# Kernel tuning notes

Measured on AMD Instinct MI355X. Metric: run time of the kernel, lower is better.

## Reference

```python
import jax, jax.numpy as jnp
import numpy as np

F0_DIM, PH_DIM, MIDI_DIM, DUR_DIM = 64, 128, 64, 64
COND = 256
TOTAL = F0_DIM + PH_DIM + MIDI_DIM + DUR_DIM  # 320
EPS = 1e-5


def setup_inputs() -> dict:
    key = jax.random.key(0)
    ks = jax.random.split(key, 16)
    B, T = 16, 4096
    inp = {
        "f0": jax.random.uniform(ks[0], (B, T), jnp.float32) * 400.0 + 80.0,
        "phone": jax.random.randint(ks[1], (B, T), 0, 100, jnp.int32),
        "duration": jax.random.uniform(ks[2], (B, T), jnp.float32),
        "midi": jax.random.randint(ks[3], (B, T), 0, 128, jnp.int32),
        # f0 encoder: Linear(1,32) -> ReLU -> Linear(32,64)
        "f0_w1": jax.random.normal(ks[4], (1, F0_DIM // 2), jnp.float32) * 0.1,
        "f0_b1": jnp.zeros((F0_DIM // 2,), jnp.float32),
        "f0_w2": jax.random.normal(ks[5], (F0_DIM // 2, F0_DIM), jnp.float32) * 0.1,
        "f0_b2": jnp.zeros((F0_DIM,), jnp.float32),
        # embeddings
        "phone_table": jax.random.normal(ks[6], (100, PH_DIM), jnp.float32),
        "midi_table": jax.random.normal(ks[7], (128, MIDI_DIM), jnp.float32),
        # duration encoder: Linear(1,32) -> ReLU -> Linear(32,64)
        "dur_w1": jax.random.normal(ks[8], (1, DUR_DIM // 2), jnp.float32) * 0.1,
        "dur_b1": jnp.zeros((DUR_DIM // 2,), jnp.float32),
        "dur_w2": jax.random.normal(ks[9], (DUR_DIM // 2, DUR_DIM), jnp.float32) * 0.1,
        "dur_b2": jnp.zeros((DUR_DIM,), jnp.float32),
        # projection: Linear(320,256) -> LayerNorm(256) -> ReLU -> Linear(256,256)
        "proj_w1": jax.random.normal(ks[10], (TOTAL, COND), jnp.float32) * (1.0 / np.sqrt(TOTAL)),
        "proj_b1": jnp.zeros((COND,), jnp.float32),
        "ln_g": jnp.ones((COND,), jnp.float32),
        "ln_b": jnp.zeros((COND,), jnp.float32),
        "proj_w2": jax.random.normal(ks[11], (COND, COND), jnp.float32) * (1.0 / np.sqrt(COND)),
        "proj_b2": jnp.zeros((COND,), jnp.float32),
    }
    return inp


def reference(f0, phone, duration, midi,
              f0_w1, f0_b1, f0_w2, f0_b2,
              phone_table, midi_table,
              dur_w1, dur_b1, dur_w2, dur_b2,
              proj_w1, proj_b1, ln_g, ln_b, proj_w2, proj_b2):
    # f0 / duration MLPs, vectorized over all (batch, time) positions
    f0_h = jax.nn.relu(f0[..., None] * f0_w1[0] + f0_b1)            # [B,T,32]
    f0_emb = f0_h @ f0_w2 + f0_b2                                    # [B,T,64]
    dur_h = jax.nn.relu(duration[..., None] * dur_w1[0] + dur_b1)    # [B,T,32]
    dur_emb = dur_h @ dur_w2 + dur_b2                                # [B,T,64]
    phone_emb = phone_table[phone]                                   # [B,T,128]
    midi_emb = midi_table[midi]                                      # [B,T,64]
    combined = jnp.concatenate([f0_emb, phone_emb, midi_emb, dur_emb], axis=-1)  # [B,T,320]
    h = combined @ proj_w1 + proj_b1                                 # [B,T,256]
    mu = jnp.mean(h, axis=-1, keepdims=True)
    var = jnp.mean((h - mu) ** 2, axis=-1, keepdims=True)
    h = (h - mu) * jax.lax.rsqrt(var + EPS) * ln_g + ln_b
    h = jax.nn.relu(h)
    return h @ proj_w2 + proj_b2                                     # [B,T,256]
```

## Files before the change

### kernel.cpp

```cpp
#include <hip/hip_runtime.h>

typedef _Float16 f16x8 __attribute__((ext_vector_type(8)));
typedef float f32x4 __attribute__((ext_vector_type(4)));
typedef unsigned int u32x2 __attribute__((ext_vector_type(2)));

#define MROWS 65536
#define BM 32
#define NBLK (MROWS / BM)

#define B1F_OFF 0u
#define B2F_OFF 65536u
#define TP_OFF 196608u
#define TM_OFF 299008u
#define BC_OFF 430080u
#define WFD_OFF 431104u


__device__ __forceinline__ unsigned a2off(unsigned X) {
  return (X * 16u) ^ (X & 0x30u);
}

__global__ __launch_bounds__(256) void prep_tables(
    const float* __restrict__ f0_w2, const float* __restrict__ f0_b2,
    const float* __restrict__ ptab, const float* __restrict__ mtab,
    const float* __restrict__ dur_w2, const float* __restrict__ dur_b2,
    const float* __restrict__ W1, const float* __restrict__ pb1,
    float* __restrict__ wsf) {
  const int r = blockIdx.x, n = threadIdx.x;
  if (r < 64) {
    float s = 0.f;
    if (r < 32) {
      for (int j = 0; j < 64; ++j) s = fmaf(f0_w2[r * 64 + j], W1[j * 256 + n], s);
    } else {
      for (int j = 0; j < 64; ++j) s = fmaf(dur_w2[(r - 32) * 64 + j], W1[(256 + j) * 256 + n], s);
    }
    wsf[WFD_OFF / 4 + r * 256 + n] = s;
  } else if (r < 164) {
    const int p = r - 64;
    float s = 0.f;
    for (int j = 0; j < 128; ++j) s = fmaf(ptab[p * 128 + j], W1[(64 + j) * 256 + n], s);
    wsf[TP_OFF / 4 + p * 256 + n] = s;
  } else if (r < 292) {
    const int m = r - 164;
    float s = 0.f;
    for (int j = 0; j < 64; ++j) s = fmaf(mtab[m * 64 + j], W1[(192 + j) * 256 + n], s);
    wsf[TM_OFF / 4 + m * 256 + n] = s;
  } else {
    float s = pb1[n];
    for (int j = 0; j < 64; ++j) {
      s = fmaf(f0_b2[j], W1[j * 256 + n], s);
      s = fmaf(dur_b2[j], W1[(256 + j) * 256 + n], s);
    }
    wsf[BC_OFF / 4 + n] = s;
  }
}

__global__ __launch_bounds__(64) void prep_frags(const float* __restrict__ W2, char* __restrict__ ws) {
  const float* Wfd = (const float*)(ws + WFD_OFF);
  const int t = blockIdx.x;
  const int l = threadIdx.x;
  const int qq = l >> 4, c = l & 15;
  if (t < 32) {
    const int kt = t >> 4, nt = t & 15;
    const int col = (nt >> 2) * 64 + c * 4 + (nt & 3);
    f16x8 v;
#pragma unroll
    for (int e = 0; e < 8; ++e) {
      const int k = kt * 32 + 4 * qq + (e & 3) + 16 * (e >> 2);
      v[e] = (_Float16)Wfd[k * 256 + col];
    }
    *(f16x8*)(ws + B1F_OFF + (unsigned)((kt * 16 + nt) * 64 + l) * 16u) = v;
  } else {
    const int t2 = t - 32;
    const int kt = t2 >> 4, nt = t2 & 15;
    const int col = (nt >> 2) * 64 + c * 4 + (nt & 3);
    f16x8 v;
#pragma unroll
    for (int e = 0; e < 8; ++e) {
      const int k = kt * 32 + 4 * qq + (e & 3) + 16 * (e >> 2);
      v[e] = (_Float16)W2[k * 256 + col];
    }
    *(f16x8*)(ws + B2F_OFF + (unsigned)((kt * 16 + nt) * 64 + l) * 16u) = v;
  }
}

__global__ __launch_bounds__(256, 4) void cond_enc_main(
    const float* __restrict__ f0g, const int* __restrict__ phone,
    const float* __restrict__ durg, const int* __restrict__ midi,
    const float* __restrict__ f0_w1, const float* __restrict__ f0_b1,
    const float* __restrict__ dur_w1, const float* __restrict__ dur_b1,
    const float* __restrict__ ln_g, const float* __restrict__ ln_b,
    const float* __restrict__ pb2, const char* __restrict__ ws,
    float* __restrict__ out) {
  __shared__ __align__(16) unsigned char smem[16384 + 512];
  unsigned char* Pbuf = smem;
  float* partials = (float*)(smem + 16384);

  const int tid = threadIdx.x;
  const int l = tid & 63;
  const int w = tid >> 6;
  const int wi = w & 1;
  const int wh = w >> 1;
  const int q = l >> 4;
  const int c = l & 15;
  const int rowbase = blockIdx.x * BM;

  const float* Tp = (const float*)(ws + TP_OFF);
  const float* Tm = (const float*)(ws + TM_OFF);

  const int rl = l & 31;
  const float xf_all = f0g[rowbase + rl];
  const float xd_all = durg[rowbase + rl];
  const int ph_all = phone[rowbase + rl];
  const int md_all = midi[rowbase + rl];

  f16x8 a1[2];
  {
    const float xf = __shfl(xf_all, wi * 16 + c);
    const float xd = __shfl(xd_all, wi * 16 + c);
#pragma unroll
    for (int kh = 0; kh < 2; ++kh) {
      f16x8 v;
#pragma unroll
      for (int e = 0; e < 8; ++e) {
        const int ki = 4 * q + (e & 3) + 16 * (e >> 2);
        const float wv = kh ? dur_w1[ki] : f0_w1[ki];
        const float bv = kh ? dur_b1[ki] : f0_b1[ki];
        const float x = kh ? xd : xf;
        v[e] = (_Float16)fmaxf(fmaf(x, wv, bv), 0.f);
      }
      a1[kh] = v;
    }
  }

  const f32x4 zero4 = {0.f, 0.f, 0.f, 0.f};
  f32x4 acc[8];
#pragma unroll
  for (int j = 0; j < 8; ++j) acc[j] = zero4;
  {
    const f16x8* B1p = (const f16x8*)(ws + B1F_OFF);
#pragma unroll
    for (int kt = 0; kt < 2; ++kt) {
#pragma unroll
      for (int jc = 0; jc < 2; ++jc) {
        f16x8 bfr[4];
#pragma unroll
        for (int j = 0; j < 4; ++j) bfr[j] = B1p[(kt * 16 + wh * 8 + jc * 4 + j) * 64 + l];
#pragma unroll
        for (int j = 0; j < 4; ++j)
          acc[jc * 4 + j] = __builtin_amdgcn_mfma_f32_16x16x32_f16(a1[kt], bfr[j], acc[jc * 4 + j], 0, 0, 0);
      }
    }
  }

  const float* bcp = (const float*)(ws + BC_OFF);
#pragma unroll
  for (int r = 0; r < 4; ++r) {
    const int rrel = wi * 16 + q * 4 + r;
    const int ph = __shfl(ph_all, rrel);
    const int md = __shfl(md_all, rrel);
    float s = 0.f, ss = 0.f;
#pragma unroll
    for (int gl = 0; gl < 2; ++gl) {
      const int g = wh * 2 + gl;
      const f32x4 tp4 = *(const f32x4*)(Tp + ph * 256 + g * 64 + c * 4);
      const f32x4 tm4 = *(const f32x4*)(Tm + md * 256 + g * 64 + c * 4);
      const f32x4 bc4 = *(const f32x4*)(bcp + g * 64 + c * 4);
#pragma unroll
      for (int bq = 0; bq < 4; ++bq) {
        float v = acc[4 * gl + bq][r] + bc4[bq] + tp4[bq] + tm4[bq];
        acc[4 * gl + bq][r] = v;
        s += v;
        ss = fmaf(v, v, ss);
      }
    }
#pragma unroll
    for (int m = 1; m < 16; m <<= 1) {
      s += __shfl_xor(s, m, 64);
      ss += __shfl_xor(ss, m, 64);
    }
    if (c == 0) {
      partials[rrel * 4 + wh * 2 + 0] = s;
      partials[rrel * 4 + wh * 2 + 1] = ss;
    }
  }
  __syncthreads();

  const int lp_base = 16 * (c & 3);
  const unsigned hoff = (unsigned)((c >> 2) & 1) * 8u;
#pragma unroll
  for (int r = 0; r < 4; ++r) {
    const int rrel = wi * 16 + q * 4 + r;
    const f32x4 pr = *(const f32x4*)(partials + rrel * 4);
    const float s = pr[0] + pr[2];
    const float ss = pr[1] + pr[3];
    const float mu = s * (1.f / 256.f);
    const float var = fmaxf(ss * (1.f / 256.f) - mu * mu, 0.f);
    const float rstd = rsqrtf(var + 1e-5f);
#pragma unroll
    for (int gl = 0; gl < 2; ++gl) {
      const int g = wh * 2 + gl;
      const f32x4 g4 = *(const f32x4*)(ln_g + g * 64 + c * 4);
      const f32x4 lb4 = *(const f32x4*)(ln_b + g * 64 + c * 4);
      unsigned short hw[4];
#pragma unroll
      for (int bq = 0; bq < 4; ++bq) {
        float v = fmaf((acc[4 * gl + bq][r] - mu) * rstd, g4[bq], lb4[bq]);
        v = fmaxf(v, 0.f);
        hw[bq] = __builtin_bit_cast(unsigned short, (_Float16)v);
      }
      u32x2 pkt;
      pkt[0] = (unsigned)hw[0] | ((unsigned)hw[1] << 16);
      pkt[1] = (unsigned)hw[2] | ((unsigned)hw[3] << 16);
      const int kt = 2 * g + (c >> 3);
      const unsigned X = (unsigned)((kt * 2 + wi) * 64 + (q * 4 + r + lp_base));
      *(u32x2*)(Pbuf + a2off(X) + hoff) = pkt;
    }
  }
  __syncthreads();

  f32x4 acc2[2][4];
#pragma unroll
  for (int i = 0; i < 2; ++i)
#pragma unroll
    for (int j = 0; j < 4; ++j) acc2[i][j] = zero4;
  {
    const f16x8* B2p = (const f16x8*)(ws + B2F_OFF);
#pragma unroll
    for (int kt = 0; kt < 8; ++kt) {
      const f16x8 a0 = *(const f16x8*)(Pbuf + a2off((unsigned)((kt * 2 + 0) * 64 + l)));
      const f16x8 a1f = *(const f16x8*)(Pbuf + a2off((unsigned)((kt * 2 + 1) * 64 + l)));
      f16x8 bfr[4];
#pragma unroll
      for (int j = 0; j < 4; ++j) bfr[j] = B2p[(kt * 16 + w * 4 + j) * 64 + l];
#pragma unroll
      for (int j = 0; j < 4; ++j) {
        acc2[0][j] = __builtin_amdgcn_mfma_f32_16x16x32_f16(a0, bfr[j], acc2[0][j], 0, 0, 0);
        acc2[1][j] = __builtin_amdgcn_mfma_f32_16x16x32_f16(a1f, bfr[j], acc2[1][j], 0, 0, 0);
      }
    }
  }

  const f32x4 b24 = *(const f32x4*)(pb2 + w * 64 + c * 4);
#pragma unroll
  for (int i = 0; i < 2; ++i)
#pragma unroll
    for (int r = 0; r < 4; ++r) {
      const int grow = rowbase + i * 16 + q * 4 + r;
      f32x4 st;
#pragma unroll
      for (int j = 0; j < 4; ++j) st[j] = acc2[i][j][r] + b24[j];
      __builtin_nontemporal_store(st, (f32x4*)(out + grow * 256 + w * 64 + c * 4));
    }
}

extern "C" void kernel_launch(void* const* d_in, const int* in_sizes, int n_in,
                              void* d_out, int out_size, void* d_ws, size_t ws_size,
                              hipStream_t stream) {
  (void)in_sizes; (void)n_in; (void)out_size; (void)ws_size;
  const float* f0 = (const float*)d_in[0];
  const int* phone = (const int*)d_in[1];
  const float* dur = (const float*)d_in[2];
  const int* midi = (const int*)d_in[3];
  const float* f0_w1 = (const float*)d_in[4];
  const float* f0_b1 = (const float*)d_in[5];
  const float* f0_w2 = (const float*)d_in[6];
  const float* f0_b2 = (const float*)d_in[7];
  const float* ptab = (const float*)d_in[8];
  const float* mtab = (const float*)d_in[9];
  const float* dur_w1 = (const float*)d_in[10];
  const float* dur_b1 = (const float*)d_in[11];
  const float* dur_w2 = (const float*)d_in[12];
  const float* dur_b2 = (const float*)d_in[13];
  const float* W1 = (const float*)d_in[14];
  const float* pb1 = (const float*)d_in[15];
  const float* ln_g = (const float*)d_in[16];
  const float* ln_b = (const float*)d_in[17];
  const float* W2 = (const float*)d_in[18];
  const float* pb2 = (const float*)d_in[19];
  char* ws = (char*)d_ws;
  float* out = (float*)d_out;

  prep_tables<<<293, 256, 0, stream>>>(f0_w2, f0_b2, ptab, mtab, dur_w2, dur_b2, W1, pb1, (float*)ws);
  prep_frags<<<160, 64, 0, stream>>>(W2, ws);
  cond_enc_main<<<NBLK, 256, 0, stream>>>(f0, phone, dur, midi, f0_w1, f0_b1, dur_w1, dur_b1,
                                          ln_g, ln_b, pb2, ws, out);
}
```

Before: 38.27 us.

## Double main-kernel row tile to 64 and split prep-table reductions across 4 warps

Result: no change. 37.87 us, median of 2 (-1.0%).

```diff
diff --git a/kernel.cpp b/kernel.cpp
--- a/kernel.cpp
+++ b/kernel.cpp
@@ -5,7 +5,7 @@
 typedef unsigned int u32x2 __attribute__((ext_vector_type(2)));
 
 #define MROWS 65536
-#define BM 32
+#define BM 64
 #define NBLK (MROWS / BM)
 
 #define B1F_OFF 0u
@@ -20,38 +20,44 @@
   return (X * 16u) ^ (X & 0x30u);
 }
 
-__global__ __launch_bounds__(256) void prep_tables(
+__global__ __launch_bounds__(1024) void prep_tables(
     const float* __restrict__ f0_w2, const float* __restrict__ f0_b2,
     const float* __restrict__ ptab, const float* __restrict__ mtab,
     const float* __restrict__ dur_w2, const float* __restrict__ dur_b2,
     const float* __restrict__ W1, const float* __restrict__ pb1,
     float* __restrict__ wsf) {
-  const int r = blockIdx.x, n = threadIdx.x;
+  __shared__ float red[4][256];
+  const int r = blockIdx.x;
+  const int n = threadIdx.x & 255;
+  const int ks = threadIdx.x >> 8;
+  float s = 0.f;
   if (r < 64) {
-    float s = 0.f;
     if (r < 32) {
-      for (int j = 0; j < 64; ++j) s = fmaf(f0_w2[r * 64 + j], W1[j * 256 + n], s);
+      for (int j = ks * 16; j < ks * 16 + 16; ++j) s = fmaf(f0_w2[r * 64 + j], W1[j * 256 + n], s);
     } else {
-      for (int j = 0; j < 64; ++j) s = fmaf(dur_w2[(r - 32) * 64 + j], W1[(256 + j) * 256 + n], s);
-    }
-    wsf[WFD_OFF / 4 + r * 256 + n] = s;
+      for (int j = ks * 16; j < ks * 16 + 16; ++j)
+        s = fmaf(dur_w2[(r - 32) * 64 + j], W1[(256 + j) * 256 + n], s);
+    }
   } else if (r < 164) {
     const int p = r - 64;
-    float s = 0.f;
-    for (int j = 0; j < 128; ++j) s = fmaf(ptab[p * 128 + j], W1[(64 + j) * 256 + n], s);
-    wsf[TP_OFF / 4 + p * 256 + n] = s;
+    for (int j = ks * 32; j < ks * 32 + 32; ++j) s = fmaf(ptab[p * 128 + j], W1[(64 + j) * 256 + n], s);
   } else if (r < 292) {
     const int m = r - 164;
-    float s = 0.f;
-    for (int j = 0; j < 64; ++j) s = fmaf(mtab[m * 64 + j], W1[(192 + j) * 256 + n], s);
-    wsf[TM_OFF / 4 + m * 256 + n] = s;
+    for (int j = ks * 16; j < ks * 16 + 16; ++j) s = fmaf(mtab[m * 64 + j], W1[(192 + j) * 256 + n], s);
   } else {
-    float s = pb1[n];
-    for (int j = 0; j < 64; ++j) {
+    for (int j = ks * 16; j < ks * 16 + 16; ++j) {
       s = fmaf(f0_b2[j], W1[j * 256 + n], s);
       s = fmaf(dur_b2[j], W1[(256 + j) * 256 + n], s);
     }
-    wsf[BC_OFF / 4 + n] = s;
+  }
+  red[ks][n] = s;
+  __syncthreads();
+  if (ks == 0) {
+    float t = red[0][n] + red[1][n] + red[2][n] + red[3][n];
+    if (r < 64) wsf[WFD_OFF / 4 + r * 256 + n] = t;
+    else if (r < 164) wsf[TP_OFF / 4 + (r - 64) * 256 + n] = t;
+    else if (r < 292) wsf[TM_OFF / 4 + (r - 164) * 256 + n] = t;
+    else wsf[BC_OFF / 4 + n] = t + pb1[n];
   }
 }
 
@@ -84,7 +90,7 @@
   }
 }
 
-__global__ __launch_bounds__(256, 4) void cond_enc_main(
+__global__ __launch_bounds__(256, 3) void cond_enc_main(
     const float* __restrict__ f0g, const int* __restrict__ phone,
     const float* __restrict__ durg, const int* __restrict__ midi,
     const float* __restrict__ f0_w1, const float* __restrict__ f0_b1,
@@ -92,9 +98,9 @@
     const float* __restrict__ ln_g, const float* __restrict__ ln_b,
     const float* __restrict__ pb2, const char* __restrict__ ws,
     float* __restrict__ out) {
-  __shared__ __align__(16) unsigned char smem[16384 + 512];
+  __shared__ __align__(16) unsigned char smem[32768 + 1024];
   unsigned char* Pbuf = smem;
-  float* partials = (float*)(smem + 16384);
+  float* partials = (float*)(smem + 32768);
 
   const int tid = threadIdx.x;
   const int l = tid & 63;
@@ -108,16 +114,16 @@
   const float* Tp = (const float*)(ws + TP_OFF);
   const float* Tm = (const float*)(ws + TM_OFF);
 
-  const int rl = l & 31;
-  const float xf_all = f0g[rowbase + rl];
-  const float xd_all = durg[rowbase + rl];
-  const int ph_all = phone[rowbase + rl];
-  const int md_all = midi[rowbase + rl];
-
-  f16x8 a1[2];
-  {
-    const float xf = __shfl(xf_all, wi * 16 + c);
-    const float xd = __shfl(xd_all, wi * 16 + c);
+  const float xf_all = f0g[rowbase + l];
+  const float xd_all = durg[rowbase + l];
+  const int ph_all = phone[rowbase + l];
+  const int md_all = midi[rowbase + l];
+
+  f16x8 a1[2][2];
+#pragma unroll
+  for (int i = 0; i < 2; ++i) {
+    const float xf = __shfl(xf_all, wi * 32 + i * 16 + c);
+    const float xd = __shfl(xd_all, wi * 32 + i * 16 + c);
 #pragma unroll
     for (int kh = 0; kh < 2; ++kh) {
       f16x8 v;
@@ -129,14 +135,16 @@
         const float x = kh ? xd : xf;
         v[e] = (_Float16)fmaxf(fmaf(x, wv, bv), 0.f);
       }
-      a1[kh] = v;
+      a1[i][kh] = v;
     }
   }
 
   const f32x4 zero4 = {0.f, 0.f, 0.f, 0.f};
-  f32x4 acc[8];
-#pragma unroll
-  for (int j = 0; j < 8; ++j) acc[j] = zero4;
+  f32x4 acc1[2][8];
+#pragma unroll
+  for (int i = 0; i < 2; ++i)
+#pragma unroll
+    for (int j = 0; j < 8; ++j) acc1[i][j] = zero4;
   {
     const f16x8* B1p = (const f16x8*)(ws + B1F_OFF);
 #pragma unroll
@@ -147,41 +155,47 @@
 #pragma unroll
         for (int j = 0; j < 4; ++j) bfr[j] = B1p[(kt * 16 + wh * 8 + jc * 4 + j) * 64 + l];
 #pragma unroll
-        for (int j = 0; j < 4; ++j)
-          acc[jc * 4 + j] = __builtin_amdgcn_mfma_f32_16x16x32_f16(a1[kt], bfr[j], acc[jc * 4 + j], 0, 0, 0);
+        for (int i = 0; i < 2; ++i)
+#pragma unroll
+          for (int j = 0; j < 4; ++j)
+            acc1[i][jc * 4 + j] =
+                __builtin_amdgcn_mfma_f32_16x16x32_f16(a1[i][kt], bfr[j], acc1[i][jc * 4 + j], 0, 0, 0);
       }
     }
   }
 
   const float* bcp = (const float*)(ws + BC_OFF);
 #pragma unroll
-  for (int r = 0; r < 4; ++r) {
-    const int rrel = wi * 16 + q * 4 + r;
-    const int ph = __shfl(ph_all, rrel);
-    const int md = __shfl(md_all, rrel);
-    float s = 0.f, ss = 0.f;
-#pragma unroll
-    for (int gl = 0; gl < 2; ++gl) {
-      const int g = wh * 2 + gl;
-      const f32x4 tp4 = *(const f32x4*)(Tp + ph * 256 + g * 64 + c * 4);
-      const f32x4 tm4 = *(const f32x4*)(Tm + md * 256 + g * 64 + c * 4);
-      const f32x4 bc4 = *(const f32x4*)(bcp + g * 64 + c * 4);
-#pragma unroll
-      for (int bq = 0; bq < 4; ++bq) {
-        float v = acc[4 * gl + bq][r] + bc4[bq] + tp4[bq] + tm4[bq];
-        acc[4 * gl + bq][r] = v;
-        s += v;
-        ss = fmaf(v, v, ss);
-      }
-    }
-#pragma unroll
-    for (int m = 1; m < 16; m <<= 1) {
-      s += __shfl_xor(s, m, 64);
-      ss += __shfl_xor(ss, m, 64);
-    }
-    if (c == 0) {
-      partials[rrel * 4 + wh * 2 + 0] = s;
-      partials[rrel * 4 + wh * 2 + 1] = ss;
+  for (int i = 0; i < 2; ++i) {
+#pragma unroll
+    for (int r = 0; r < 4; ++r) {
+      const int rrel = wi * 32 + i * 16 + q * 4 + r;
+      const int ph = __shfl(ph_all, rrel);
+      const int md = __shfl(md_all, rrel);
+      float s = 0.f, ss = 0.f;
+#pragma unroll
+      for (int gl = 0; gl < 2; ++gl) {
+        const int g = wh * 2 + gl;
+        const f32x4 tp4 = *(const f32x4*)(Tp + ph * 256 + g * 64 + c * 4);
+        const f32x4 tm4 = *(const f32x4*)(Tm + md * 256 + g * 64 + c * 4);
+        const f32x4 bc4 = *(const f32x4*)(bcp + g * 64 + c * 4);
+#pragma unroll
+        for (int bq = 0; bq < 4; ++bq) {
+          float v = acc1[i][4 * gl + bq][r] + bc4[bq] + tp4[bq] + tm4[bq];
+          acc1[i][4 * gl + bq][r] = v;
+          s += v;
+          ss = fmaf(v, v, ss);
+        }
+      }
+#pragma unroll
+      for (int m = 1; m < 16; m <<= 1) {
+        s += __shfl_xor(s, m, 64);
+        ss += __shfl_xor(ss, m, 64);
+      }
+      if (c == 0) {
+        partials[rrel * 4 + wh * 2 + 0] = s;
+        partials[rrel * 4 + wh * 2 + 1] = ss;
+      }
     }
   }
   __syncthreads();
@@ -189,67 +203,72 @@
   const int lp_base = 16 * (c & 3);
   const unsigned hoff = (unsigned)((c >> 2) & 1) * 8u;
 #pragma unroll
-  for (int r = 0; r < 4; ++r) {
-    const int rrel = wi * 16 + q * 4 + r;
-    const f32x4 pr = *(const f32x4*)(partials + rrel * 4);
-    const float s = pr[0] + pr[2];
-    const float ss = pr[1] + pr[3];
-    const float mu = s * (1.f / 256.f);
-    const float var = fmaxf(ss * (1.f / 256.f) - mu * mu, 0.f);
-    const float rstd = rsqrtf(var + 1e-5f);
-#pragma unroll
-    for (int gl = 0; gl < 2; ++gl) {
-      const int g = wh * 2 + gl;
-      const f32x4 g4 = *(const f32x4*)(ln_g + g * 64 + c * 4);
-      const f32x4 lb4 = *(const f32x4*)(ln_b + g * 64 + c * 4);
-      unsigned short hw[4];
-#pragma unroll
-      for (int bq = 0; bq < 4; ++bq) {
-        float v = fmaf((acc[4 * gl + bq][r] - mu) * rstd, g4[bq], lb4[bq]);
-        v = fmaxf(v, 0.f);
-        hw[bq] = __builtin_bit_cast(unsigned short, (_Float16)v);
-      }
-      u32x2 pkt;
-      pkt[0] = (unsigned)hw[0] | ((unsigned)hw[1] << 16);
-      pkt[1] = (unsigned)hw[2] | ((unsigned)hw[3] << 16);
-      const int kt = 2 * g + (c >> 3);
-      const unsigned X = (unsigned)((kt * 2 + wi) * 64 + (q * 4 + r + lp_base));
-      *(u32x2*)(Pbuf + a2off(X) + hoff) = pkt;
+  for (int i = 0; i < 2; ++i) {
+#pragma unroll
+    for (int r = 0; r < 4; ++r) {
+      const int rrel = wi * 32 + i * 16 + q * 4 + r;
+      const int it = wi * 2 + i;
+      const f32x4 pr = *(const f32x4*)(partials + rrel * 4);
+      const float s = pr[0] + pr[2];
+      const float ss = pr[1] + pr[3];
+      const float mu = s * (1.f / 256.f);
+      const float var = fmaxf(ss * (1.f / 256.f) - mu * mu, 0.f);
+      const float rstd = rsqrtf(var + 1e-5f);
+#pragma unroll
+      for (int gl = 0; gl < 2; ++gl) {
+        const int g = wh * 2 + gl;
+        const f32x4 g4 = *(const f32x4*)(ln_g + g * 64 + c * 4);
+        const f32x4 lb4 = *(const f32x4*)(ln_b + g * 64 + c * 4);
+        unsigned short hw[4];
+#pragma unroll
+        for (int bq = 0; bq < 4; ++bq) {
+          float v = fmaf((acc1[i][4 * gl + bq][r] - mu) * rstd, g4[bq], lb4[bq]);
+          v = fmaxf(v, 0.f);
+          hw[bq] = __builtin_bit_cast(unsigned short, (_Float16)v);
+        }
+        u32x2 pkt;
+        pkt[0] = (unsigned)hw[0] | ((unsigned)hw[1] << 16);
+        pkt[1] = (unsigned)hw[2] | ((unsigned)hw[3] << 16);
+        const int kt = 2 * g + (c >> 3);
+        const unsigned X = (unsigned)((kt * 4 + it) * 64 + (q * 4 + r + lp_base));
+        *(u32x2*)(Pbuf + a2off(X) + hoff) = pkt;
+      }
     }
   }
   __syncthreads();
 
-  f32x4 acc2[2][4];
-#pragma unroll
-  for (int i = 0; i < 2; ++i)
-#pragma unroll
-    for (int j = 0; j < 4; ++j) acc2[i][j] = zero4;
+  f32x4 acc2[4][4];
+#pragma unroll
+  for (int it = 0; it < 4; ++it)
+#pragma unroll
+    for (int j = 0; j < 4; ++j) acc2[it][j] = zero4;
   {
     const f16x8* B2p = (const f16x8*)(ws + B2F_OFF);
 #pragma unroll
     for (int kt = 0; kt < 8; ++kt) {
-      const f16x8 a0 = *(const f16x8*)(Pbuf + a2off((unsigned)((kt * 2 + 0) * 64 + l)));
-      const f16x8 a1f = *(const f16x8*)(Pbuf + a2off((unsigned)((kt * 2 + 1) * 64 + l)));
-      f16x8 bfr[4];
+      f16x8 av[4], bfr[4];
+#pragma unroll
+      for (int it = 0; it < 4; ++it)
+        av[it] = *(const f16x8*)(Pbuf + a2off((unsigned)((kt * 4 + it) * 64 + l)));
 #pragma unroll
       for (int j = 0; j < 4; ++j) bfr[j] = B2p[(kt * 16 + w * 4 + j) * 64 + l];
 #pragma unroll
-      for (int j = 0; j < 4; ++j) {
-        acc2[0][j] = __builtin_amdgcn_mfma_f32_16x16x32_f16(a0, bfr[j], acc2[0][j], 0, 0, 0);
-        acc2[1][j] = __builtin_amdgcn_mfma_f32_16x16x32_f16(a1f, bfr[j], acc2[1][j], 0, 0, 0);
-      }
+      for (int it = 0; it < 4; ++it)
+#pragma unroll
+        for (int j = 0; j < 4; ++j)
+          acc2[it][j] = __builtin_amdgcn_mfma_f32_16x16x32_f16(av[it], bfr[j], acc2[it][j], 0, 0, 0);
     }
   }
 
   const f32x4 b24 = *(const f32x4*)(pb2 + w * 64 + c * 4);
 #pragma unroll
-  for (int i = 0; i < 2; ++i)
+  for (int it = 0; it < 4; ++it)
 #pragma unroll
     for (int r = 0; r < 4; ++r) {
-      const int grow = rowbase + i * 16 + q * 4 + r;
+      const int grow = rowbase + it * 16 + q * 4 + r;
       f32x4 st;
 #pragma unroll
-      for (int j = 0; j < 4; ++j) st[j] = acc2[i][j][r] + b24[j];
+      for (int j = 0; j < 4; ++j) st[j] = acc2[it][j][r] + b24[j];
       __builtin_nontemporal_store(st, (f32x4*)(out + grow * 256 + w * 64 + c * 4));
     }
 }
@@ -281,7 +300,7 @@
   char* ws = (char*)d_ws;
   float* out = (float*)d_out;
 
-  prep_tables<<<293, 256, 0, stream>>>(f0_w2, f0_b2, ptab, mtab, dur_w2, dur_b2, W1, pb1, (float*)ws);
+  prep_tables<<<293, 1024, 0, stream>>>(f0_w2, f0_b2, ptab, mtab, dur_w2, dur_b2, W1, pb1, (float*)ws);
   prep_frags<<<160, 64, 0, stream>>>(W2, ws);
   cond_enc_main<<<NBLK, 256, 0, stream>>>(f0, phone, dur, midi, f0_w1, f0_b1, dur_w1, dur_b1,
                                           ln_g, ln_b, pb2, ws, out);
```
